# Kernel optimization log

Hardware: AMD Instinct MI355X
Metric: run time of the kernel (lower is better)

Reference implementation:

```python
import jax, jax.numpy as jnp
import numpy as np

B, T, E, A = 8, 2048, 1024, 1024


def setup_inputs() -> dict:
    key = jax.random.key(0)
    k1, k2, k3, k4 = jax.random.split(key, 4)
    embedded = jax.random.normal(k1, (B, T, E), dtype=jnp.float32)
    s = 1.0 / np.sqrt(E)
    # nn.Linear(E, A, bias=False) stores weight of shape (A, E); y = x @ W^T
    Wq = jax.random.uniform(k2, (A, E), dtype=jnp.float32, minval=-s, maxval=s)
    Wk = jax.random.uniform(k3, (A, E), dtype=jnp.float32, minval=-s, maxval=s)
    Wv = jax.random.uniform(k4, (A, E), dtype=jnp.float32, minval=-s, maxval=s)
    return {"embedded": embedded, "Wq": Wq, "Wk": Wk, "Wv": Wv}


def reference(embedded, Wq, Wk, Wv):
    # q, k, v: [B, T, A]
    q = jnp.einsum("bte,ae->bta", embedded, Wq)
    k = jnp.einsum("bte,ae->bta", embedded, Wk)
    v = jnp.einsum("bte,ae->bta", embedded, Wv)
    scale = 1.0 / jnp.sqrt(jnp.asarray(Wq.shape[0], dtype=q.dtype))
    # causal scores: [B, T, T]
    scores = jnp.einsum("bqa,bka->bqk", q, k) * scale
    t = scores.shape[-1]
    causal = jnp.tril(jnp.ones((t, t), dtype=bool))
    scores = jnp.where(causal, scores, jnp.asarray(-jnp.inf, dtype=scores.dtype))
    attn = jax.nn.softmax(scores, axis=-1)
    return jnp.einsum("bqk,bka->bqa", attn, v)
```

## Files before the change

kernel.cpp:

```cpp
#include <hip/hip_runtime.h>
#include <hip/hip_bf16.h>
#include <stdint.h>


#define BB 8
#define TT 2048
#define EE 1024
#define AA 1024
#define MM (BB * TT)

typedef short bf16x8 __attribute__((ext_vector_type(8)));
typedef float f32x4 __attribute__((ext_vector_type(4)));

#define GLOAD_LDS16(g, l)                                                      \
  __builtin_amdgcn_global_load_lds(                                            \
      (const __attribute__((address_space(1))) void*)(g),                      \
      (__attribute__((address_space(3))) void*)(l), 16, 0, 0)

#define SBAR()                               \
  do {                                       \
    __builtin_amdgcn_sched_barrier(0);       \
    __builtin_amdgcn_s_barrier();            \
    __builtin_amdgcn_sched_barrier(0);       \
  } while (0)

#define LGKM0()                                          \
  do {                                                   \
    asm volatile("s_waitcnt lgkmcnt(0)" ::: "memory");   \
    __builtin_amdgcn_sched_barrier(0);                   \
  } while (0)

#define VMCNT(n)                                              \
  do {                                                        \
    asm volatile("s_waitcnt vmcnt(" #n ")" ::: "memory");     \
    __builtin_amdgcn_sched_barrier(0);                        \
  } while (0)

__device__ __forceinline__ void gemm256_core(
    const short* __restrict__ gA, int lda, int a0row,
    const short* __restrict__ gB, int ldb, int b0row, int NT, short* As,
    short* Bs, f32x4 (*acc)[4]) {
  const int tid = threadIdx.x;
  const int lane = tid & 63;
  const int w = tid >> 6;
  const int wr = w >> 2, wc = w & 3;
  const int lrow = lane & 15;
  const int lk8 = (lane >> 4) * 8;
  const int swz = ((lrow >> 3) & 1) << 4;
  const int baseA = (((wr * 128 + lrow) * 32) + lk8) ^ swz;
  const int baseB = (((wc * 64 + lrow) * 32) + lk8) ^ swz;

  const short* pA[2];
  const short* pB[2];
  int dL[2];
#pragma unroll
  for (int i = 0; i < 2; ++i) {
    int chunk = 2 * w + i;
    int P = chunk * 1024 + lane * 16;
    int L = P ^ (((P >> 9) & 1) << 5);
    int row = L >> 6;
    int kb2 = (L & 63) >> 1;
    pA[i] = gA + (size_t)(a0row + row) * lda + kb2;
    pB[i] = gB + (size_t)(b0row + row) * ldb + kb2;
    dL[i] = chunk * 512 + lane * 8;
  }

#define STG_A(tl, s)                                                           \
  do {                                                                         \
    int _o = (tl) * 64 + (s) * 32;                                             \
    short* _d = As + (((tl) & 1) << 14) + ((s) << 13);                         \
    GLOAD_LDS16(pA[0] + _o, _d + dL[0]);                                       \
    GLOAD_LDS16(pA[1] + _o, _d + dL[1]);                                       \
  } while (0)
#define STG_B(tl, s)                                                           \
  do {                                                                         \
    int _o = (tl) * 64 + (s) * 32;                                             \
    short* _d = Bs + (((tl) & 1) << 14) + ((s) << 13);                         \
    GLOAD_LDS16(pB[0] + _o, _d + dL[0]);                                       \
    GLOAD_LDS16(pB[1] + _o, _d + dL[1]);                                       \
  } while (0)

  STG_B(0, 0); STG_A(0, 0); STG_B(0, 1); STG_A(0, 1);
  if (NT > 1) {
    STG_B(1, 0); STG_A(1, 0); STG_A(1, 1);
    VMCNT(6);
  } else {
    VMCNT(0);
  }
  SBAR();

  for (int t = 0; t < NT; ++t) {
    short* Ac = As + (t & 1) * 16384;
    short* Bc = Bs + (t & 1) * 16384;
    const bool stg = (t < NT - 2);
    bf16x8 a0[4], a1[4], a2[4], a3[4], b0[4], b1[4];

#pragma unroll
    for (int m = 0; m < 4; ++m) a0[m] = *(const bf16x8*)&Ac[baseA + m * 512];
#pragma unroll
    for (int n = 0; n < 4; ++n) b0[n] = *(const bf16x8*)&Bc[baseB + n * 512];
    if (t < NT - 1) STG_B(t + 1, 1);
    SBAR();
    LGKM0();
    __builtin_amdgcn_s_setprio(1);
#pragma unroll
    for (int m = 0; m < 4; ++m)
#pragma unroll
      for (int n = 0; n < 4; ++n)
        acc[m][n] = __builtin_amdgcn_mfma_f32_16x16x32_bf16(a0[m], b0[n],
                                                            acc[m][n], 0, 0, 0);
    __builtin_amdgcn_s_setprio(0);
    SBAR();

#pragma unroll
    for (int m = 0; m < 4; ++m)
      a1[m] = *(const bf16x8*)&Ac[baseA + (m + 4) * 512];
#pragma unroll
    for (int m = 0; m < 4; ++m)
      a2[m] = *(const bf16x8*)&Ac[8192 + baseA + m * 512];
    if (stg) STG_B(t + 2, 0);
    SBAR();
    LGKM0();
    __builtin_amdgcn_s_setprio(1);
#pragma unroll
    for (int m = 0; m < 4; ++m)
#pragma unroll
      for (int n = 0; n < 4; ++n)
        acc[m + 4][n] = __builtin_amdgcn_mfma_f32_16x16x32_bf16(
            a1[m], b0[n], acc[m + 4][n], 0, 0, 0);
    __builtin_amdgcn_s_setprio(0);
    SBAR();

#pragma unroll
    for (int m = 0; m < 4; ++m)
      a3[m] = *(const bf16x8*)&Ac[8192 + baseA + (m + 4) * 512];
#pragma unroll
    for (int n = 0; n < 4; ++n)
      b1[n] = *(const bf16x8*)&Bc[8192 + baseB + n * 512];
    if (stg) STG_A(t + 2, 0);
    SBAR();
    LGKM0();
    __builtin_amdgcn_s_setprio(1);
#pragma unroll
    for (int m = 0; m < 4; ++m)
#pragma unroll
      for (int n = 0; n < 4; ++n)
        acc[m][n] = __builtin_amdgcn_mfma_f32_16x16x32_bf16(a2[m], b1[n],
                                                            acc[m][n], 0, 0, 0);
    __builtin_amdgcn_s_setprio(0);
    SBAR();

    if (stg) {
      STG_A(t + 2, 1);
      VMCNT(6);
    } else if (t == NT - 2) {
      VMCNT(0);
    }
    SBAR();
    __builtin_amdgcn_s_setprio(1);
#pragma unroll
    for (int m = 0; m < 4; ++m)
#pragma unroll
      for (int n = 0; n < 4; ++n)
        acc[m + 4][n] = __builtin_amdgcn_mfma_f32_16x16x32_bf16(
            a3[m], b1[n], acc[m + 4][n], 0, 0, 0);
    __builtin_amdgcn_s_setprio(0);
    SBAR();
  }
#undef STG_A
#undef STG_B
}

__device__ __forceinline__ void stage_tile(const short* __restrict__ g,
                                           size_t stride, short* lds, int tid) {
#pragma unroll
  for (int r = 0; r < 4; ++r) {
    int t = r * 256 + tid;
    int row = t >> 3;
    int c = (t & 7) * 8;
    GLOAD_LDS16(g + (size_t)row * stride + c, lds + (size_t)t * 8);
  }
}

__device__ __forceinline__ void mfma_step(const short* As, const short* Bs,
                                          f32x4 acc[4][4], int lane, int wr,
                                          int wc) {
  int lrow = lane & 15;
  int lk = (lane >> 4) * 8;
#pragma unroll
  for (int kk = 0; kk < 64; kk += 32) {
    bf16x8 a[4], b[4];
#pragma unroll
    for (int i = 0; i < 4; ++i)
      a[i] = *(const bf16x8*)&As[(wr * 64 + i * 16 + lrow) * 64 + kk + lk];
#pragma unroll
    for (int j = 0; j < 4; ++j)
      b[j] = *(const bf16x8*)&Bs[(wc * 64 + j * 16 + lrow) * 64 + kk + lk];
#pragma unroll
    for (int i = 0; i < 4; ++i)
#pragma unroll
      for (int j = 0; j < 4; ++j)
        acc[i][j] =
            __builtin_amdgcn_mfma_f32_16x16x32_bf16(a[i], b[j], acc[i][j], 0, 0, 0);
  }
}

__global__ __launch_bounds__(512, 2) void qkv_gemm8(
    const short* __restrict__ xb, const short* __restrict__ Wb,
    short* __restrict__ qk, short* __restrict__ Vt) {
  __shared__ __align__(16) short SH[65536];
  short* As = SH;
  short* Bs = SH + 32768;
  int f = blockIdx.x;
  int s = (f & 7) * 96 + (f >> 3);
  int mt = s / 12, nt = s % 12;
  int z = nt >> 2, ntl = nt & 3;
  const short* gB = Wb + (size_t)z * AA * EE + (size_t)(ntl * 256) * EE;
  f32x4 acc[8][4];
#pragma unroll
  for (int m = 0; m < 8; ++m)
#pragma unroll
    for (int n = 0; n < 4; ++n) acc[m][n] = (f32x4){0.f, 0.f, 0.f, 0.f};
  gemm256_core(xb, EE, mt * 256, gB, EE, 0, EE / 64, As, Bs, acc);

  int tid = threadIdx.x;
  int lane = tid & 63, w = tid >> 6, wr = w >> 2, wc = w & 3;
  int lrow = lane & 15, lk4 = (lane >> 4) * 4;

  if (z < 2) {
    short* o = qk + (size_t)z * MM * AA;
    int row0 = mt * 256 + wr * 128;
    int col0 = ntl * 256 + wc * 64;
#pragma unroll
    for (int m = 0; m < 8; ++m)
#pragma unroll
      for (int n = 0; n < 4; ++n)
#pragma unroll
        for (int r = 0; r < 4; ++r) {
          int row = row0 + m * 16 + lk4 + r;
          int col = col0 + n * 16 + lrow;
          __hip_bfloat16 h = __float2bfloat16(acc[m][n][r]);
          o[(size_t)row * AA + col] = *(short*)&h;
        }
  } else {
    __syncthreads();
    int lr0 = wr * 128, lc0 = wc * 64;
#pragma unroll
    for (int m = 0; m < 8; ++m)
#pragma unroll
      for (int n = 0; n < 4; ++n)
#pragma unroll
        for (int r = 0; r < 4; ++r) {
          int lr = lr0 + m * 16 + lk4 + r;
          int lc = lc0 + n * 16 + lrow;
          __hip_bfloat16 h = __float2bfloat16(acc[m][n][r]);
          SH[lc * 256 + (lr ^ ((lc & 7) << 3))] = *(short*)&h;
        }
    __syncthreads();
    int row0 = mt * 256;
    int bq = row0 >> 11;
    int t0 = row0 & 2047;
#pragma unroll
    for (int pass = 0; pass < 4; ++pass) {
      int lc = pass * 64 + (tid >> 3);
      int d = ntl * 256 + lc;
      size_t dst = ((size_t)bq * AA + d) * TT + t0;
      int sw = (lc & 7) << 3;
#pragma unroll
      for (int g = 0; g < 4; ++g) {
        int lr = (tid & 7) * 8 + g * 64;
        bf16x8 vv = *(const bf16x8*)&SH[lc * 256 + (lr ^ sw)];
        *(bf16x8*)&Vt[dst + lr] = vv;
      }
    }
  }
}

__global__ __launch_bounds__(512, 2) void score_fused(
    const short* __restrict__ Qb, const short* __restrict__ Kb,
    short* __restrict__ Pu, float* __restrict__ lsum) {
  __shared__ __align__(16) short As[32768];
  __shared__ __align__(16) short Bs[32768];
  int f = blockIdx.x;
  int b = f & 7;
  int j = f >> 3;
  int MT = 1;
  while ((MT + 1) * MT / 2 <= j) ++MT;
  int NT = j - MT * (MT - 1) / 2;
  const short* Q = Qb + (size_t)b * TT * AA;
  const short* K = Kb + (size_t)b * TT * AA;
  const float scale = 0.03125f;
  short* P = Pu + (size_t)b * TT * TT;
  int tid = threadIdx.x;

  {
    f32x4 acc[8][4];
#pragma unroll
    for (int m = 0; m < 8; ++m)
#pragma unroll
      for (int n = 0; n < 4; ++n) acc[m][n] = (f32x4){0.f, 0.f, 0.f, 0.f};
    gemm256_core(Q, AA, MT * 256, K, AA, NT * 256, AA / 64, As, Bs, acc);

    int lane = tid & 63, w = tid >> 6, wr = w >> 2, wc = w & 3;
    int lrow = lane & 15, lk4 = (lane >> 4) * 4;
    int q0 = MT * 256 + wr * 128;
    int c0 = NT * 256 + wc * 64;
#pragma unroll
    for (int m = 0; m < 8; ++m) {
#pragma unroll
      for (int r = 0; r < 4; ++r) {
        int q = q0 + m * 16 + lk4 + r;
        float rs = 0.f;
#pragma unroll
        for (int n = 0; n < 4; ++n) {
          int kx = c0 + n * 16 + lrow;
          float e = __expf(acc[m][n][r] * scale);
          rs += e;
          __hip_bfloat16 h = __float2bfloat16(e);
          P[(size_t)q * TT + kx] = *(short*)&h;
        }
        rs += __shfl_xor(rs, 1);
        rs += __shfl_xor(rs, 2);
        rs += __shfl_xor(rs, 4);
        rs += __shfl_xor(rs, 8);
        if (lrow == 0) atomicAdd(&lsum[b * TT + q], rs);
      }
    }
  }

  if (j < 24) {
    int M = j / 3, r3 = j - 3 * M;
    int mt = 2 * M + (r3 > 0);
    int nt = 2 * M + (r3 == 2);
    int q0 = mt * 128, c0 = nt * 128;
    bool act = tid < 256;
    int lane = tid & 63, wid = (tid >> 6) & 3, wr = wid >> 1, wc = wid & 1;
    int lrow = lane & 15, lk4 = (lane >> 4) * 4;

    f32x4 acc[4][4];
#pragma unroll
    for (int i = 0; i < 4; ++i)
#pragma unroll
      for (int jj = 0; jj < 4; ++jj) acc[i][jj] = (f32x4){0.f, 0.f, 0.f, 0.f};

    __syncthreads();
    for (int k0 = 0; k0 < AA; k0 += 64) {
      if (act) {
        stage_tile(Q + (size_t)q0 * AA + k0, AA, As, tid);
        stage_tile(K + (size_t)c0 * AA + k0, AA, Bs, tid);
      }
      __syncthreads();
      if (act) mfma_step(As, Bs, acc, lane, wr, wc);
      __syncthreads();
    }
    if (act) {
#pragma unroll
      for (int i = 0; i < 4; ++i) {
#pragma unroll
        for (int r = 0; r < 4; ++r) {
          int q = q0 + wr * 64 + i * 16 + lk4 + r;
          float rs = 0.f;
#pragma unroll
          for (int jj = 0; jj < 4; ++jj) {
            int kx = c0 + wc * 64 + jj * 16 + lrow;
            float e = (kx <= q) ? __expf(acc[i][jj][r] * scale) : 0.f;
            rs += e;
            __hip_bfloat16 h = __float2bfloat16(e);
            P[(size_t)q * TT + kx] = *(short*)&h;
          }
          rs += __shfl_xor(rs, 1);
          rs += __shfl_xor(rs, 2);
          rs += __shfl_xor(rs, 4);
          rs += __shfl_xor(rs, 8);
          if (lrow == 0) atomicAdd(&lsum[b * TT + q], rs);
        }
      }
    }
  }
}

__global__ __launch_bounds__(256) void pv_gemm(const short* __restrict__ Pu,
                                               const short* __restrict__ Vt,
                                               const float* __restrict__ lsum,
                                               float* __restrict__ out) {
  int f = blockIdx.x;
  int b = f & 7;
  int j = f >> 3;
  int p = j >> 3;
  int nt = j & 7;
  int n0 = nt * 128;

  __shared__ __align__(16) short As[128 * 64];
  __shared__ __align__(16) short Bs[128 * 64];
  int tid = threadIdx.x;
  int lane = tid & 63, wid = tid >> 6, wr = wid >> 1, wc = wid & 1;
  const short* P = Pu + (size_t)b * TT * TT;
  const short* V = Vt + (size_t)b * AA * TT;
  int lrow = lane & 15, lk4 = (lane >> 4) * 4;

#pragma unroll
  for (int s = 0; s < 2; ++s) {
    int mt = s ? (15 - p) : p;
    int q0 = mt * 128;
    f32x4 acc[4][4];
#pragma unroll
    for (int i = 0; i < 4; ++i)
#pragma unroll
      for (int jj = 0; jj < 4; ++jj) acc[i][jj] = (f32x4){0.f, 0.f, 0.f, 0.f};

    int kend = q0 + 128;
    for (int k0 = 0; k0 < kend; k0 += 64) {
      stage_tile(P + (size_t)q0 * TT + k0, TT, As, tid);
      stage_tile(V + (size_t)n0 * TT + k0, TT, Bs, tid);
      __syncthreads();
      mfma_step(As, Bs, acc, lane, wr, wc);
      __syncthreads();
    }
#pragma unroll
    for (int i = 0; i < 4; ++i) {
#pragma unroll
      for (int r = 0; r < 4; ++r) {
        int q = q0 + wr * 64 + i * 16 + lk4 + r;
        float linv = 1.0f / lsum[b * TT + q];
#pragma unroll
        for (int jj = 0; jj < 4; ++jj) {
          int d = n0 + wc * 64 + jj * 16 + lrow;
          out[((size_t)(b * TT + q)) * AA + d] = acc[i][jj][r] * linv;
        }
      }
    }
  }
}

__global__ void prep(const float* __restrict__ x, const float* __restrict__ wq,
                     const float* __restrict__ wk, const float* __restrict__ wv,
                     short* __restrict__ Xb, short* __restrict__ Wb,
                     float* __restrict__ Ls) {
  const int nx4 = MM * EE / 4;
  const int nw4 = AA * EE / 4;
  int gid = blockIdx.x * blockDim.x + threadIdx.x;
  if (gid < MM) Ls[gid] = 0.f;
  int stride = gridDim.x * blockDim.x;
  for (int i = gid; i < nx4 + 3 * nw4; i += stride) {
    const float* src;
    short* dst;
    int ii;
    if (i < nx4) {
      src = x; dst = Xb; ii = i;
    } else {
      int j = i - nx4;
      int z = j / nw4;
      ii = j - z * nw4;
      src = (z == 0) ? wq : (z == 1 ? wk : wv);
      dst = Wb + (size_t)z * AA * EE;
    }
    float4 v = ((const float4*)src)[ii];
    __hip_bfloat16 h0 = __float2bfloat16(v.x);
    __hip_bfloat16 h1 = __float2bfloat16(v.y);
    __hip_bfloat16 h2 = __float2bfloat16(v.z);
    __hip_bfloat16 h3 = __float2bfloat16(v.w);
    short4 o;
    o.x = *(short*)&h0;
    o.y = *(short*)&h1;
    o.z = *(short*)&h2;
    o.w = *(short*)&h3;
    ((short4*)dst)[ii] = o;
  }
}

extern "C" void kernel_launch(void* const* d_in, const int* in_sizes, int n_in,
                              void* d_out, int out_size, void* d_ws,
                              size_t ws_size, hipStream_t stream) {
  const float* x = (const float*)d_in[0];
  const float* Wq = (const float*)d_in[1];
  const float* Wk = (const float*)d_in[2];
  const float* Wv = (const float*)d_in[3];

  char* ws = (char*)d_ws;
  size_t oWb = 0;
  size_t oQb = oWb + (size_t)3 * AA * EE * 2;
  size_t oKb = oQb + (size_t)MM * AA * 2;
  size_t oVt = oKb + (size_t)MM * AA * 2;
  size_t oLs = oVt + (size_t)MM * AA * 2;
  size_t oXb = oLs + (size_t)MM * 4;
  size_t oPu = oXb;

  short* Wb = (short*)(ws + oWb);
  short* Qb = (short*)(ws + oQb);
  short* Kb = (short*)(ws + oKb);
  short* Vt = (short*)(ws + oVt);
  float* Ls = (float*)(ws + oLs);
  short* Xb = (short*)(ws + oXb);
  short* Pu = (short*)(ws + oPu);

  prep<<<2048, 256, 0, stream>>>(x, Wq, Wk, Wv, Xb, Wb, Ls);

  qkv_gemm8<<<768, 512, 0, stream>>>(Xb, Wb, Qb, Vt);
  score_fused<<<224, 512, 0, stream>>>(Qb, Kb, Pu, Ls);
  pv_gemm<<<512, 256, 0, stream>>>(Pu, Vt, Ls, (float*)d_out);
}
```

Before: 248.1 us.

## Move V projection into score kernel to fill idle CUs alongside score tiles

The fused QKV GEMM is split: the first kernel now computes only Q and K (512 blocks), and the V projection with its transpose is moved into the score kernel as 256 extra blocks running beside the 224 causal score blocks. The goal is to use CUs that the 224-block score launch leaves idle, and to shorten the QKV kernel's tail. P no longer aliases the Xb buffer, because Xb is still read during the score kernel, so the workspace grows. Mixing heterogeneous block types in one grid can create imbalance depending on scheduling order.

```diff
diff --git a/kernel.cpp b/kernel.cpp
--- a/kernel.cpp
+++ b/kernel.cpp
@@ -205,16 +205,17 @@
   }
 }
 
-__global__ __launch_bounds__(512, 2) void qkv_gemm8(
+__global__ __launch_bounds__(512, 2) void qkv_qk(
     const short* __restrict__ xb, const short* __restrict__ Wb,
-    short* __restrict__ qk, short* __restrict__ Vt) {
+    short* __restrict__ qk) {
   __shared__ __align__(16) short SH[65536];
   short* As = SH;
   short* Bs = SH + 32768;
   int f = blockIdx.x;
-  int s = (f & 7) * 96 + (f >> 3);
-  int mt = s / 12, nt = s % 12;
-  int z = nt >> 2, ntl = nt & 3;
+  int s = (f & 7) * 64 + (f >> 3);
+  int mt = s >> 3;
+  int rem = s & 7;
+  int z = rem >> 2, ntl = rem & 3;
   const short* gB = Wb + (size_t)z * AA * EE + (size_t)(ntl * 256) * EE;
   f32x4 acc[8][4];
 #pragma unroll
@@ -226,25 +227,141 @@
   int tid = threadIdx.x;
   int lane = tid & 63, w = tid >> 6, wr = w >> 2, wc = w & 3;
   int lrow = lane & 15, lk4 = (lane >> 4) * 4;
-
-  if (z < 2) {
-    short* o = qk + (size_t)z * MM * AA;
-    int row0 = mt * 256 + wr * 128;
-    int col0 = ntl * 256 + wc * 64;
+  short* o = qk + (size_t)z * MM * AA;
+  int row0 = mt * 256 + wr * 128;
+  int col0 = ntl * 256 + wc * 64;
+#pragma unroll
+  for (int m = 0; m < 8; ++m)
+#pragma unroll
+    for (int n = 0; n < 4; ++n)
+#pragma unroll
+      for (int r = 0; r < 4; ++r) {
+        int row = row0 + m * 16 + lk4 + r;
+        int col = col0 + n * 16 + lrow;
+        __hip_bfloat16 h = __float2bfloat16(acc[m][n][r]);
+        o[(size_t)row * AA + col] = *(short*)&h;
+      }
+}
+
+__global__ __launch_bounds__(512, 2) void score_v(
+    const short* __restrict__ xb, const short* __restrict__ Wb,
+    const short* __restrict__ Qb, const short* __restrict__ Kb,
+    short* __restrict__ Pu, float* __restrict__ lsum,
+    short* __restrict__ Vt) {
+  __shared__ __align__(16) short SH[65536];
+  short* As = SH;
+  short* Bs = SH + 32768;
+  int f = blockIdx.x;
+  int tid = threadIdx.x;
+  int lane = tid & 63, w = tid >> 6, wr8 = w >> 2, wc8 = w & 3;
+  int lrow = lane & 15, lk4 = (lane >> 4) * 4;
+  const float scale = 0.03125f;
+
+  if (f < 224) {
+    int b = f & 7;
+    int j = f >> 3;
+    int MT = 1;
+    while ((MT + 1) * MT / 2 <= j) ++MT;
+    int NT = j - MT * (MT - 1) / 2;
+    const short* Q = Qb + (size_t)b * TT * AA;
+    const short* K = Kb + (size_t)b * TT * AA;
+    short* P = Pu + (size_t)b * TT * TT;
+
+    {
+      f32x4 acc[8][4];
+#pragma unroll
+      for (int m = 0; m < 8; ++m)
+#pragma unroll
+        for (int n = 0; n < 4; ++n) acc[m][n] = (f32x4){0.f, 0.f, 0.f, 0.f};
+      gemm256_core(Q, AA, MT * 256, K, AA, NT * 256, AA / 64, As, Bs, acc);
+
+      int q0 = MT * 256 + wr8 * 128;
+      int c0 = NT * 256 + wc8 * 64;
+#pragma unroll
+      for (int m = 0; m < 8; ++m) {
+#pragma unroll
+        for (int r = 0; r < 4; ++r) {
+          int q = q0 + m * 16 + lk4 + r;
+          float rs = 0.f;
+#pragma unroll
+          for (int n = 0; n < 4; ++n) {
+            int kx = c0 + n * 16 + lrow;
+            float e = __expf(acc[m][n][r] * scale);
+            rs += e;
+            __hip_bfloat16 h = __float2bfloat16(e);
+            P[(size_t)q * TT + kx] = *(short*)&h;
+          }
+          rs += __shfl_xor(rs, 1);
+          rs += __shfl_xor(rs, 2);
+          rs += __shfl_xor(rs, 4);
+          rs += __shfl_xor(rs, 8);
+          if (lrow == 0) atomicAdd(&lsum[b * TT + q], rs);
+        }
+      }
+    }
+
+    if (j < 24) {
+      int M = j / 3, r3 = j - 3 * M;
+      int mt = 2 * M + (r3 > 0);
+      int nt = 2 * M + (r3 == 2);
+      int q0 = mt * 128, c0 = nt * 128;
+      bool act = tid < 256;
+      int wid4 = (tid >> 6) & 3, wr = wid4 >> 1, wc = wid4 & 1;
+
+      f32x4 acc[4][4];
+#pragma unroll
+      for (int i = 0; i < 4; ++i)
+#pragma unroll
+        for (int jj = 0; jj < 4; ++jj) acc[i][jj] = (f32x4){0.f, 0.f, 0.f, 0.f};
+
+      __syncthreads();
+      for (int k0 = 0; k0 < AA; k0 += 64) {
+        if (act) {
+          stage_tile(Q + (size_t)q0 * AA + k0, AA, As, tid);
+          stage_tile(K + (size_t)c0 * AA + k0, AA, Bs, tid);
+        }
+        __syncthreads();
+        if (act) mfma_step(As, Bs, acc, lane, wr, wc);
+        __syncthreads();
+      }
+      if (act) {
+#pragma unroll
+        for (int i = 0; i < 4; ++i) {
+#pragma unroll
+          for (int r = 0; r < 4; ++r) {
+            int q = q0 + wr * 64 + i * 16 + lk4 + r;
+            float rs = 0.f;
+#pragma unroll
+            for (int jj = 0; jj < 4; ++jj) {
+              int kx = c0 + wc * 64 + jj * 16 + lrow;
+              float e = (kx <= q) ? __expf(acc[i][jj][r] * scale) : 0.f;
+              rs += e;
+              __hip_bfloat16 h = __float2bfloat16(e);
+              P[(size_t)q * TT + kx] = *(short*)&h;
+            }
+            rs += __shfl_xor(rs, 1);
+            rs += __shfl_xor(rs, 2);
+            rs += __shfl_xor(rs, 4);
+            rs += __shfl_xor(rs, 8);
+            if (lrow == 0) atomicAdd(&lsum[b * TT + q], rs);
+          }
+        }
+      }
+    }
+  } else {
+    int g = f - 224;
+    int s2 = (g & 7) * 32 + (g >> 3);
+    int mt = s2 >> 2, ntl = s2 & 3;
+    const short* gB = Wb + (size_t)2 * AA * EE + (size_t)(ntl * 256) * EE;
+    f32x4 acc[8][4];
 #pragma unroll
     for (int m = 0; m < 8; ++m)
 #pragma unroll
-      for (int n = 0; n < 4; ++n)
-#pragma unroll
-        for (int r = 0; r < 4; ++r) {
-          int row = row0 + m * 16 + lk4 + r;
-          int col = col0 + n * 16 + lrow;
-          __hip_bfloat16 h = __float2bfloat16(acc[m][n][r]);
-          o[(size_t)row * AA + col] = *(short*)&h;
-        }
-  } else {
+      for (int n = 0; n < 4; ++n) acc[m][n] = (f32x4){0.f, 0.f, 0.f, 0.f};
+    gemm256_core(xb, EE, mt * 256, gB, EE, 0, EE / 64, As, Bs, acc);
+
     __syncthreads();
-    int lr0 = wr * 128, lc0 = wc * 64;
+    int lr0 = wr8 * 128, lc0 = wc8 * 64;
 #pragma unroll
     for (int m = 0; m < 8; ++m)
 #pragma unroll
@@ -267,113 +384,10 @@
       size_t dst = ((size_t)bq * AA + d) * TT + t0;
       int sw = (lc & 7) << 3;
 #pragma unroll
-      for (int g = 0; g < 4; ++g) {
-        int lr = (tid & 7) * 8 + g * 64;
+      for (int gg = 0; gg < 4; ++gg) {
+        int lr = (tid & 7) * 8 + gg * 64;
         bf16x8 vv = *(const bf16x8*)&SH[lc * 256 + (lr ^ sw)];
         *(bf16x8*)&Vt[dst + lr] = vv;
-      }
-    }
-  }
-}
-
-__global__ __launch_bounds__(512, 2) void score_fused(
-    const short* __restrict__ Qb, const short* __restrict__ Kb,
-    short* __restrict__ Pu, float* __restrict__ lsum) {
-  __shared__ __align__(16) short As[32768];
-  __shared__ __align__(16) short Bs[32768];
-  int f = blockIdx.x;
-  int b = f & 7;
-  int j = f >> 3;
-  int MT = 1;
-  while ((MT + 1) * MT / 2 <= j) ++MT;
-  int NT = j - MT * (MT - 1) / 2;
-  const short* Q = Qb + (size_t)b * TT * AA;
-  const short* K = Kb + (size_t)b * TT * AA;
-  const float scale = 0.03125f;
-  short* P = Pu + (size_t)b * TT * TT;
-  int tid = threadIdx.x;
-
-  {
-    f32x4 acc[8][4];
-#pragma unroll
-    for (int m = 0; m < 8; ++m)
-#pragma unroll
-      for (int n = 0; n < 4; ++n) acc[m][n] = (f32x4){0.f, 0.f, 0.f, 0.f};
-    gemm256_core(Q, AA, MT * 256, K, AA, NT * 256, AA / 64, As, Bs, acc);
-
-    int lane = tid & 63, w = tid >> 6, wr = w >> 2, wc = w & 3;
-    int lrow = lane & 15, lk4 = (lane >> 4) * 4;
-    int q0 = MT * 256 + wr * 128;
-    int c0 = NT * 256 + wc * 64;
-#pragma unroll
-    for (int m = 0; m < 8; ++m) {
-#pragma unroll
-      for (int r = 0; r < 4; ++r) {
-        int q = q0 + m * 16 + lk4 + r;
-        float rs = 0.f;
-#pragma unroll
-        for (int n = 0; n < 4; ++n) {
-          int kx = c0 + n * 16 + lrow;
-          float e = __expf(acc[m][n][r] * scale);
-          rs += e;
-          __hip_bfloat16 h = __float2bfloat16(e);
-          P[(size_t)q * TT + kx] = *(short*)&h;
-        }
-        rs += __shfl_xor(rs, 1);
-        rs += __shfl_xor(rs, 2);
-        rs += __shfl_xor(rs, 4);
-        rs += __shfl_xor(rs, 8);
-        if (lrow == 0) atomicAdd(&lsum[b * TT + q], rs);
-      }
-    }
-  }
-
-  if (j < 24) {
-    int M = j / 3, r3 = j - 3 * M;
-    int mt = 2 * M + (r3 > 0);
-    int nt = 2 * M + (r3 == 2);
-    int q0 = mt * 128, c0 = nt * 128;
-    bool act = tid < 256;
-    int lane = tid & 63, wid = (tid >> 6) & 3, wr = wid >> 1, wc = wid & 1;
-    int lrow = lane & 15, lk4 = (lane >> 4) * 4;
-
-    f32x4 acc[4][4];
-#pragma unroll
-    for (int i = 0; i < 4; ++i)
-#pragma unroll
-      for (int jj = 0; jj < 4; ++jj) acc[i][jj] = (f32x4){0.f, 0.f, 0.f, 0.f};
-
-    __syncthreads();
-    for (int k0 = 0; k0 < AA; k0 += 64) {
-      if (act) {
-        stage_tile(Q + (size_t)q0 * AA + k0, AA, As, tid);
-        stage_tile(K + (size_t)c0 * AA + k0, AA, Bs, tid);
-      }
-      __syncthreads();
-      if (act) mfma_step(As, Bs, acc, lane, wr, wc);
-      __syncthreads();
-    }
-    if (act) {
-#pragma unroll
-      for (int i = 0; i < 4; ++i) {
-#pragma unroll
-        for (int r = 0; r < 4; ++r) {
-          int q = q0 + wr * 64 + i * 16 + lk4 + r;
-          float rs = 0.f;
-#pragma unroll
-          for (int jj = 0; jj < 4; ++jj) {
-            int kx = c0 + wc * 64 + jj * 16 + lrow;
-            float e = (kx <= q) ? __expf(acc[i][jj][r] * scale) : 0.f;
-            rs += e;
-            __hip_bfloat16 h = __float2bfloat16(e);
-            P[(size_t)q * TT + kx] = *(short*)&h;
-          }
-          rs += __shfl_xor(rs, 1);
-          rs += __shfl_xor(rs, 2);
-          rs += __shfl_xor(rs, 4);
-          rs += __shfl_xor(rs, 8);
-          if (lrow == 0) atomicAdd(&lsum[b * TT + q], rs);
-        }
       }
     }
   }
@@ -483,7 +497,7 @@
   size_t oVt = oKb + (size_t)MM * AA * 2;
   size_t oLs = oVt + (size_t)MM * AA * 2;
   size_t oXb = oLs + (size_t)MM * 4;
-  size_t oPu = oXb;
+  size_t oPu = oXb + (size_t)MM * EE * 2;
 
   short* Wb = (short*)(ws + oWb);
   short* Qb = (short*)(ws + oQb);
@@ -495,7 +509,7 @@
 
   prep<<<2048, 256, 0, stream>>>(x, Wq, Wk, Wv, Xb, Wb, Ls);
 
-  qkv_gemm8<<<768, 512, 0, stream>>>(Xb, Wb, Qb, Vt);
-  score_fused<<<224, 512, 0, stream>>>(Qb, Kb, Pu, Ls);
+  qkv_qk<<<512, 512, 0, stream>>>(Xb, Wb, Qb);
+  score_v<<<480, 512, 0, stream>>>(Xb, Wb, Qb, Kb, Pu, Ls, Vt);
   pv_gemm<<<512, 256, 0, stream>>>(Pu, Vt, Ls, (float*)d_out);
 }
```

Measured after the change: 244.8 us (median of 3 runs). No clear change (-1.3%).
